# Performance work log

Hardware: AMD Instinct MI355X
Metric: run time of the kernel (lower is better)

## Reference

```python
import jax, jax.numpy as jnp
import numpy as np
import math

B, S, D, H = 4, 2048, 1024, 16
HD = D // H  # 64
SCALE = math.sqrt(HD)  # scale=True -> sqrt(d_model // n_head)

def setup_inputs() -> dict:
    key = jax.random.key(0)
    k1, k2, k3, k4, k5 = jax.random.split(key, 5)
    x = jax.random.normal(k1, (B, S, D), dtype=jnp.float32)
    char_ids = jax.random.randint(k2, (B, S), 0, 21128)
    seq_len = jax.random.randint(k3, (B,), 1, S)
    mask = jnp.ones((B, S), dtype=jnp.int64)
    W_qkv = jax.random.normal(k4, (D, 3 * D), dtype=jnp.float32) * (1.0 / math.sqrt(D))
    W_fc = jax.random.normal(k5, (D, D), dtype=jnp.float32) * (1.0 / math.sqrt(D))
    b_fc = jnp.zeros((D,), dtype=jnp.float32)
    return {"x": x, "char_ids": char_ids, "seq_len": seq_len, "mask": mask,
            "W_qkv": W_qkv, "W_fc": W_fc, "b_fc": b_fc}

def reference(x, char_ids, seq_len, mask, W_qkv, W_fc, b_fc):
    b, s, d = x.shape
    qkv = x @ W_qkv                      # [b, s, 3d]
    q, k, v = jnp.split(qkv, 3, axis=-1)
    # [b, h, s, hd]
    q = q.reshape(b, s, H, HD).transpose(0, 2, 1, 3)
    k = k.reshape(b, s, H, HD).transpose(0, 2, 1, 3)
    v = v.reshape(b, s, H, HD).transpose(0, 2, 1, 3)
    attn = jnp.einsum('bhqd,bhkd->bhqk', q, k) / SCALE
    attn = jnp.where(mask[:, None, None, :] == 0, -jnp.inf, attn)
    attn = jax.nn.softmax(attn, axis=-1)
    # dropout is identity in eval mode
    out = jnp.einsum('bhqk,bhkd->bhqd', attn, v)
    out = out.transpose(0, 2, 1, 3).reshape(b, s, d)
    return out @ W_fc + b_fc
```

## Files before the change

### kernel.cpp

```cpp
#include <hip/hip_runtime.h>
#include <hip/hip_bf16.h>


#define S_ 2048
#define D_ 1024

typedef __attribute__((ext_vector_type(4))) float f32x4;
typedef __attribute__((ext_vector_type(16))) float f32x16;
typedef __attribute__((ext_vector_type(8))) short bf16x8;

__device__ __forceinline__ unsigned short f2b(float f) {
  union { float f; unsigned u; } x; x.f = f;
  unsigned r = x.u + 0x7fffu + ((x.u >> 16) & 1u);
  return (unsigned short)(r >> 16);
}
__device__ __forceinline__ float b2f(unsigned short u) {
  union { unsigned u; float f; } x; x.u = ((unsigned)u) << 16; return x.f;
}

__device__ __forceinline__ void gload_lds16(const void* g, void* l) {
  __builtin_amdgcn_global_load_lds(
      (const __attribute__((address_space(1))) unsigned int*)g,
      (__attribute__((address_space(3))) unsigned int*)l, 16, 0, 0);
}

__global__ void cvt_f32_bf16(const float* __restrict__ in, unsigned short* __restrict__ out, int n) {
  int i = (blockIdx.x * blockDim.x + threadIdx.x) * 8;
  if (i >= n) return;
  float4 a = *(const float4*)&in[i];
  float4 b = *(const float4*)&in[i + 4];
  unsigned short r[8];
  r[0] = f2b(a.x); r[1] = f2b(a.y); r[2] = f2b(a.z); r[3] = f2b(a.w);
  r[4] = f2b(b.x); r[5] = f2b(b.y); r[6] = f2b(b.z); r[7] = f2b(b.w);
  *(uint4*)&out[i] = *(uint4*)r;
}

__global__ void transpose_cvt(const float* __restrict__ W, unsigned short* __restrict__ Wt,
                              int K, int N) {
  __shared__ unsigned short tile[32][33];
  int n0 = blockIdx.x * 32, k0 = blockIdx.y * 32;
  int tx = threadIdx.x & 31, ty = threadIdx.x >> 5;
  #pragma unroll
  for (int i = 0; i < 32; i += 8)
    tile[ty + i][tx] = f2b(W[(size_t)(k0 + ty + i) * N + n0 + tx]);
  __syncthreads();
  #pragma unroll
  for (int i = 0; i < 32; i += 8)
    Wt[(size_t)(n0 + ty + i) * K + k0 + tx] = tile[tx][ty + i];
}

template <int GY>
__global__ __launch_bounds__(256) void gemm_bt(const unsigned short* __restrict__ A,
                                               const unsigned short* __restrict__ Bt,
                                               const float* __restrict__ bias,
                                               float* __restrict__ Cf,
                                               unsigned short* __restrict__ Cb,
                                               int M, int N, int K) {
  __shared__ unsigned short As[128 * 32];
  __shared__ unsigned short Bs[128 * 32];
  int tid = threadIdx.x, wave = tid >> 6, lane = tid & 63;

  int lin = blockIdx.y * 64 + blockIdx.x;
  const int q = (GY * 64) >> 3;
  int swz = (lin & 7) * q + (lin >> 3);
  int bm = swz / GY, bn = swz % GY;

  int wr = (wave >> 1) * 64, wc = (wave & 1) * 64;
  f32x4 acc[4][4] = {};

  const unsigned short* aG0 = A + (size_t)(bm * 128 + wave * 32 + (lane >> 2)) * K + (lane & 3) * 8;
  const unsigned short* aG1 = aG0 + (size_t)16 * K;
  const unsigned short* bG0 = Bt + (size_t)(bn * 128 + wave * 32 + (lane >> 2)) * K + (lane & 3) * 8;
  const unsigned short* bG1 = bG0 + (size_t)16 * K;
  unsigned short* aL0 = As + wave * 32 * 32;
  unsigned short* aL1 = aL0 + 16 * 32;
  unsigned short* bL0 = Bs + wave * 32 * 32;
  unsigned short* bL1 = bL0 + 16 * 32;

  for (int k0 = 0; k0 < K; k0 += 32) {
    gload_lds16(aG0, aL0); gload_lds16(aG1, aL1);
    gload_lds16(bG0, bL0); gload_lds16(bG1, bL1);
    aG0 += 32; aG1 += 32; bG0 += 32; bG1 += 32;
    __syncthreads();
    bf16x8 af[4], bf[4];
    #pragma unroll
    for (int i = 0; i < 4; i++)
      af[i] = *(const bf16x8*)&As[(wr + i * 16 + (lane & 15)) * 32 + (lane >> 4) * 8];
    #pragma unroll
    for (int i = 0; i < 4; i++)
      bf[i] = *(const bf16x8*)&Bs[(wc + i * 16 + (lane & 15)) * 32 + (lane >> 4) * 8];
    #pragma unroll
    for (int i = 0; i < 4; i++)
      #pragma unroll
      for (int j = 0; j < 4; j++)
        acc[i][j] = __builtin_amdgcn_mfma_f32_16x16x32_bf16(af[i], bf[j], acc[i][j], 0, 0, 0);
    __syncthreads();
  }

  int row0 = bm * 128 + wr + (lane >> 4) * 4;
  int col0 = bn * 128 + wc + (lane & 15);
  if (Cb) {
    #pragma unroll
    for (int i = 0; i < 4; i++)
      #pragma unroll
      for (int j = 0; j < 4; j++)
        #pragma unroll
        for (int q2 = 0; q2 < 4; q2++)
          Cb[(size_t)(row0 + i * 16 + q2) * N + col0 + j * 16] = f2b(acc[i][j][q2]);
  } else {
    #pragma unroll
    for (int i = 0; i < 4; i++)
      #pragma unroll
      for (int j = 0; j < 4; j++) {
        float bv = bias[col0 + j * 16];
        #pragma unroll
        for (int q2 = 0; q2 < 4; q2++)
          Cf[(size_t)(row0 + i * 16 + q2) * N + col0 + j * 16] = acc[i][j][q2] + bv;
      }
  }
}

__global__ __launch_bounds__(256) void flash_attn(const unsigned short* __restrict__ qkv,
                                                  unsigned short* __restrict__ ao) {
  __shared__ unsigned short Ks[2][4096];
  __shared__ unsigned short Vs[2][4096];
  int tid = threadIdx.x, wave = tid >> 6, lane = tid & 63;
  int l31 = lane & 31, hi = lane >> 5;
  int bh = blockIdx.x, b = bh >> 4, h = bh & 15;
  const unsigned short* base = qkv + (size_t)b * S_ * 3072 + h * 64;
  const unsigned short* kb = base + 1024;
  const unsigned short* vb = base + 2048;
  int q0 = blockIdx.y * 256 + wave * 32;

  bf16x8 qfA[4], qfB[4];
  {
    const unsigned short* qpA = base + (size_t)(q0 + l31) * 3072 + hi * 8;
    const unsigned short* qpB = qpA + (size_t)128 * 3072;
    #pragma unroll
    for (int ks = 0; ks < 4; ks++) {
      bf16x8 va = *(const bf16x8*)(qpA + ks * 16);
      bf16x8 vc = *(const bf16x8*)(qpB + ks * 16);
      #pragma unroll
      for (int e = 0; e < 8; e++) {
        va[e] = (short)f2b(0.125f * b2f((unsigned short)va[e]));
        vc[e] = (short)f2b(0.125f * b2f((unsigned short)vc[e]));
      }
      qfA[ks] = va; qfB[ks] = vc;
    }
  }

  f32x16 oA0 = {}, oA1 = {}, oB0 = {}, oB1 = {};
  float miA = -1e30f, liA = 0.f, miB = -1e30f, liB = 0.f;

  int r_l = lane >> 3;
  int gsrc = (lane & 7) ^ r_l;
  size_t koffA = (size_t)((wave * 2 + 0) * 8 + r_l) * 3072 + gsrc * 8;
  size_t koffB = (size_t)((wave * 2 + 1) * 8 + r_l) * 3072 + gsrc * 8;
  int kvp = (tid & 31) * 2, dgr = (tid >> 5) * 8;
  int vslot = kvp >> 3;
  int vlo = kvp & 7;
  bf16x8 vr0, vr1;


  {
    gload_lds16(kb + koffA, &Ks[0][(wave * 2 + 0) * 512]);
    gload_lds16(kb + koffB, &Ks[0][(wave * 2 + 1) * 512]);
    const unsigned short* vsrc = vb + (size_t)kvp * 3072 + dgr;
    vr0 = *(const bf16x8*)vsrc;
    vr1 = *(const bf16x8*)(vsrc + 3072);
    union { bf16x8 v; unsigned u[4]; } a0, a1;
    a0.v = vr0; a1.v = vr1;
    #pragma unroll
    for (int i = 0; i < 4; i++) {
      int d0 = dgr + 2 * i, d1 = d0 + 1;
      unsigned we = (a0.u[i] & 0xffffu) | (a1.u[i] << 16);
      unsigned wo = (a0.u[i] >> 16) | (a1.u[i] & 0xffff0000u);
      *(unsigned*)&Vs[0][d0 * 64 + ((vslot ^ (d0 & 7)) << 3) + vlo] = we;
      *(unsigned*)&Vs[0][d1 * 64 + ((vslot ^ (d1 & 7)) << 3) + vlo] = wo;
    }
    __syncthreads();
  }

  for (int t = 0; t < 32; ++t) {
    int cur = t & 1;
    int tn = (t + 1) & 31;
    {
      const unsigned short* ksrc = kb + (size_t)tn * 64 * 3072;
      gload_lds16(ksrc + koffA, &Ks[cur ^ 1][(wave * 2 + 0) * 512]);
      gload_lds16(ksrc + koffB, &Ks[cur ^ 1][(wave * 2 + 1) * 512]);
      const unsigned short* vsrc = vb + (size_t)(tn * 64 + kvp) * 3072 + dgr;
      vr0 = *(const bf16x8*)vsrc;
      vr1 = *(const bf16x8*)(vsrc + 3072);
    }

    const unsigned short* Kc = Ks[cur];
    const unsigned short* Vc = Vs[cur];

    #pragma unroll
    for (int sub = 0; sub < 2; ++sub) {
      f32x16 sA = {}, sB = {};
      __builtin_amdgcn_s_setprio(1);
      #pragma unroll
      for (int ks = 0; ks < 4; ks++) {
        int row = sub * 32 + l31;
        bf16x8 kf = *(const bf16x8*)&Kc[row * 64 + ((((ks << 1) + hi) ^ (row & 7)) << 3)];
        sA = __builtin_amdgcn_mfma_f32_32x32x16_bf16(kf, qfA[ks], sA, 0, 0, 0);
        sB = __builtin_amdgcn_mfma_f32_32x32x16_bf16(kf, qfB[ks], sB, 0, 0, 0);
      }
      __builtin_amdgcn_s_setprio(0);

      union { unsigned u[4]; bf16x8 v; } PA0, PA1;
      {
        float t0 = fmaxf(fmaxf(sA[0], sA[1]), sA[2]);
        float t1 = fmaxf(fmaxf(sA[3], sA[4]), sA[5]);
        float t2 = fmaxf(fmaxf(sA[6], sA[7]), sA[8]);
        float t3 = fmaxf(fmaxf(sA[9], sA[10]), sA[11]);
        float t4 = fmaxf(fmaxf(sA[12], sA[13]), sA[14]);
        float tm = fmaxf(fmaxf(fmaxf(t0, t1), t2), fmaxf(fmaxf(t3, t4), sA[15]));
        tm = fmaxf(tm, __shfl_xor(tm, 32, 64));
        if (__any(tm > miA + 8.f)) {
          float tnew = fmaxf(miA, tm);
          float fac = __expf(miA - tnew);
          liA *= fac; miA = tnew;
          #pragma unroll
          for (int r = 0; r < 16; r++) { oA0[r] *= fac; oA1[r] *= fac; }
        }
        float p[16];
        float rs = 0.f;
        #pragma unroll
        for (int r = 0; r < 16; r++) { p[r] = __expf(sA[r] - miA); rs += p[r]; }
        liA += rs;
        unsigned c0, c1, c2, c3, c4, c5, c6, c7;
        asm("v_cvt_pk_bf16_f32 %0, %1, %2" : "=v"(c0) : "v"(p[0]),  "v"(p[1]));
        asm("v_cvt_pk_bf16_f32 %0, %1, %2" : "=v"(c1) : "v"(p[2]),  "v"(p[3]));
        asm("v_cvt_pk_bf16_f32 %0, %1, %2" : "=v"(c2) : "v"(p[4]),  "v"(p[5]));
        asm("v_cvt_pk_bf16_f32 %0, %1, %2" : "=v"(c3) : "v"(p[6]),  "v"(p[7]));
        asm("v_cvt_pk_bf16_f32 %0, %1, %2" : "=v"(c4) : "v"(p[8]),  "v"(p[9]));
        asm("v_cvt_pk_bf16_f32 %0, %1, %2" : "=v"(c5) : "v"(p[10]), "v"(p[11]));
        asm("v_cvt_pk_bf16_f32 %0, %1, %2" : "=v"(c6) : "v"(p[12]), "v"(p[13]));
        asm("v_cvt_pk_bf16_f32 %0, %1, %2" : "=v"(c7) : "v"(p[14]), "v"(p[15]));
        asm volatile("v_permlane32_swap_b32 %0, %1" : "+v"(c0), "+v"(c2));
        asm volatile("v_permlane32_swap_b32 %0, %1" : "+v"(c1), "+v"(c3));
        asm volatile("v_permlane32_swap_b32 %0, %1" : "+v"(c4), "+v"(c6));
        asm volatile("v_permlane32_swap_b32 %0, %1" : "+v"(c5), "+v"(c7));
        PA0.u[0] = c0; PA0.u[1] = c1; PA0.u[2] = c2; PA0.u[3] = c3;
        PA1.u[0] = c4; PA1.u[1] = c5; PA1.u[2] = c6; PA1.u[3] = c7;
      }
      union { unsigned u[4]; bf16x8 v; } PB0, PB1;
      {
        float t0 = fmaxf(fmaxf(sB[0], sB[1]), sB[2]);
        float t1 = fmaxf(fmaxf(sB[3], sB[4]), sB[5]);
        float t2 = fmaxf(fmaxf(sB[6], sB[7]), sB[8]);
        float t3 = fmaxf(fmaxf(sB[9], sB[10]), sB[11]);
        float t4 = fmaxf(fmaxf(sB[12], sB[13]), sB[14]);
        float tm = fmaxf(fmaxf(fmaxf(t0, t1), t2), fmaxf(fmaxf(t3, t4), sB[15]));
        tm = fmaxf(tm, __shfl_xor(tm, 32, 64));
        if (__any(tm > miB + 8.f)) {
          float tnew = fmaxf(miB, tm);
          float fac = __expf(miB - tnew);
          liB *= fac; miB = tnew;
          #pragma unroll
          for (int r = 0; r < 16; r++) { oB0[r] *= fac; oB1[r] *= fac; }
        }
        float p[16];
        float rs = 0.f;
        #pragma unroll
        for (int r = 0; r < 16; r++) { p[r] = __expf(sB[r] - miB); rs += p[r]; }
        liB += rs;
        unsigned c0, c1, c2, c3, c4, c5, c6, c7;
        asm("v_cvt_pk_bf16_f32 %0, %1, %2" : "=v"(c0) : "v"(p[0]),  "v"(p[1]));
        asm("v_cvt_pk_bf16_f32 %0, %1, %2" : "=v"(c1) : "v"(p[2]),  "v"(p[3]));
        asm("v_cvt_pk_bf16_f32 %0, %1, %2" : "=v"(c2) : "v"(p[4]),  "v"(p[5]));
        asm("v_cvt_pk_bf16_f32 %0, %1, %2" : "=v"(c3) : "v"(p[6]),  "v"(p[7]));
        asm("v_cvt_pk_bf16_f32 %0, %1, %2" : "=v"(c4) : "v"(p[8]),  "v"(p[9]));
        asm("v_cvt_pk_bf16_f32 %0, %1, %2" : "=v"(c5) : "v"(p[10]), "v"(p[11]));
        asm("v_cvt_pk_bf16_f32 %0, %1, %2" : "=v"(c6) : "v"(p[12]), "v"(p[13]));
        asm("v_cvt_pk_bf16_f32 %0, %1, %2" : "=v"(c7) : "v"(p[14]), "v"(p[15]));
        asm volatile("v_permlane32_swap_b32 %0, %1" : "+v"(c0), "+v"(c2));
        asm volatile("v_permlane32_swap_b32 %0, %1" : "+v"(c1), "+v"(c3));
        asm volatile("v_permlane32_swap_b32 %0, %1" : "+v"(c4), "+v"(c6));
        asm volatile("v_permlane32_swap_b32 %0, %1" : "+v"(c5), "+v"(c7));
        PB0.u[0] = c0; PB0.u[1] = c1; PB0.u[2] = c2; PB0.u[3] = c3;
        PB1.u[0] = c4; PB1.u[1] = c5; PB1.u[2] = c6; PB1.u[3] = c7;
      }

      int slot0 = (sub << 2) + hi;
      int slot1 = (sub << 2) + 2 + hi;
      bf16x8 v00 = *(const bf16x8*)&Vc[l31 * 64 + ((slot0 ^ (l31 & 7)) << 3)];
      bf16x8 v01 = *(const bf16x8*)&Vc[(32 + l31) * 64 + ((slot0 ^ (l31 & 7)) << 3)];
      bf16x8 v10 = *(const bf16x8*)&Vc[l31 * 64 + ((slot1 ^ (l31 & 7)) << 3)];
      bf16x8 v11 = *(const bf16x8*)&Vc[(32 + l31) * 64 + ((slot1 ^ (l31 & 7)) << 3)];
      __builtin_amdgcn_s_setprio(1);
      oA0 = __builtin_amdgcn_mfma_f32_32x32x16_bf16(v00, PA0.v, oA0, 0, 0, 0);
      oB0 = __builtin_amdgcn_mfma_f32_32x32x16_bf16(v00, PB0.v, oB0, 0, 0, 0);
      oA1 = __builtin_amdgcn_mfma_f32_32x32x16_bf16(v01, PA0.v, oA1, 0, 0, 0);
      oB1 = __builtin_amdgcn_mfma_f32_32x32x16_bf16(v01, PB0.v, oB1, 0, 0, 0);
      oA0 = __builtin_amdgcn_mfma_f32_32x32x16_bf16(v10, PA1.v, oA0, 0, 0, 0);
      oB0 = __builtin_amdgcn_mfma_f32_32x32x16_bf16(v10, PB1.v, oB0, 0, 0, 0);
      oA1 = __builtin_amdgcn_mfma_f32_32x32x16_bf16(v11, PA1.v, oA1, 0, 0, 0);
      oB1 = __builtin_amdgcn_mfma_f32_32x32x16_bf16(v11, PB1.v, oB1, 0, 0, 0);
      __builtin_amdgcn_s_setprio(0);
    }

    {
      unsigned short* Vd = Vs[cur ^ 1];
      union { bf16x8 v; unsigned u[4]; } a0, a1;
      a0.v = vr0; a1.v = vr1;
      #pragma unroll
      for (int i = 0; i < 4; i++) {
        int d0 = dgr + 2 * i, d1 = d0 + 1;
        unsigned we = (a0.u[i] & 0xffffu) | (a1.u[i] << 16);
        unsigned wo = (a0.u[i] >> 16) | (a1.u[i] & 0xffff0000u);
        *(unsigned*)&Vd[d0 * 64 + ((vslot ^ (d0 & 7)) << 3) + vlo] = we;
        *(unsigned*)&Vd[d1 * 64 + ((vslot ^ (d1 & 7)) << 3) + vlo] = wo;
      }
    }
    __syncthreads();
  }

  liA += __shfl_xor(liA, 32, 64);
  liB += __shfl_xor(liB, 32, 64);
  float invA = 1.f / liA, invB = 1.f / liB;
  unsigned short* aopA = ao + (size_t)(b * S_ + q0 + l31) * D_ + h * 64;
  unsigned short* aopB = aopA + (size_t)128 * D_;
  #pragma unroll
  for (int g = 0; g < 4; g++) {
    union { unsigned short s[4]; uint2 u; } wa0, wa1, wb0, wb1;
    #pragma unroll
    for (int e = 0; e < 4; e++) {
      wa0.s[e] = f2b(oA0[g * 4 + e] * invA);
      wa1.s[e] = f2b(oA1[g * 4 + e] * invA);
      wb0.s[e] = f2b(oB0[g * 4 + e] * invB);
      wb1.s[e] = f2b(oB1[g * 4 + e] * invB);
    }
    int d = g * 8 + hi * 4;
    *(uint2*)&aopA[d] = wa0.u;
    *(uint2*)&aopA[32 + d] = wa1.u;
    *(uint2*)&aopB[d] = wb0.u;
    *(uint2*)&aopB[32 + d] = wb1.u;
  }
}

extern "C" void kernel_launch(void* const* d_in, const int* in_sizes, int n_in,
                              void* d_out, int out_size, void* d_ws, size_t ws_size,
                              hipStream_t stream) {
  const float* x    = (const float*)d_in[0];
  const float* Wqkv = (const float*)d_in[4];
  const float* Wfc  = (const float*)d_in[5];
  const float* bfc  = (const float*)d_in[6];
  float* out = (float*)d_out;

  char* ws = (char*)d_ws;
  unsigned short* xb    = (unsigned short*)(ws);
  unsigned short* qkv   = (unsigned short*)(ws + 16777216);
  unsigned short* ao    = (unsigned short*)(ws + 67108864);
  unsigned short* wqkvT = (unsigned short*)(ws + 83886080);
  unsigned short* wfcT  = (unsigned short*)(ws + 90177536);

  cvt_f32_bf16<<<dim3(4096), dim3(256), 0, stream>>>(x, xb, 8388608);
  transpose_cvt<<<dim3(96, 32), dim3(256), 0, stream>>>(Wqkv, wqkvT, 1024, 3072);
  transpose_cvt<<<dim3(32, 32), dim3(256), 0, stream>>>(Wfc, wfcT, 1024, 1024);
  gemm_bt<24><<<dim3(64, 24), dim3(256), 0, stream>>>(xb, wqkvT, nullptr, nullptr, qkv, 8192, 3072, 1024);
  flash_attn<<<dim3(64, 8), dim3(256), 0, stream>>>(qkv, ao);
  gemm_bt<8><<<dim3(64, 8), dim3(256), 0, stream>>>(ao, wfcT, bfc, out, nullptr, 8192, 1024, 1024);
}
```

Measured before the change: 223.8 us.

## Split attention KV range across two wave groups and merge partial softmax states

The flash attention block grows to 512 threads. Two groups of four waves each process half of the key/value sequence for the same query rows, and their partial outputs and max/sum statistics are combined through shared memory at the end. Softmax exponentials now use exp2 with a prescaled max. The GEMM drops its tile-order swizzle in favour of plain blockIdx mapping, which may hurt L2 locality. The aim is more waves in flight per query tile and a shorter serial KV loop, at the cost of twice the LDS per block and an extra merge step.

After: 410.9 us. +83.6%, slower.

```diff
diff --git a/kernel.cpp b/kernel.cpp
--- a/kernel.cpp
+++ b/kernel.cpp
@@ -49,7 +49,6 @@
     Wt[(size_t)(n0 + ty + i) * K + k0 + tx] = tile[tx][ty + i];
 }
 
-template <int GY>
 __global__ __launch_bounds__(256) void gemm_bt(const unsigned short* __restrict__ A,
                                                const unsigned short* __restrict__ Bt,
                                                const float* __restrict__ bias,
@@ -59,12 +58,7 @@
   __shared__ unsigned short As[128 * 32];
   __shared__ unsigned short Bs[128 * 32];
   int tid = threadIdx.x, wave = tid >> 6, lane = tid & 63;
-
-  int lin = blockIdx.y * 64 + blockIdx.x;
-  const int q = (GY * 64) >> 3;
-  int swz = (lin & 7) * q + (lin >> 3);
-  int bm = swz / GY, bn = swz % GY;
-
+  int bm = blockIdx.x, bn = blockIdx.y;
   int wr = (wave >> 1) * 64, wc = (wave & 1) * 64;
   f32x4 acc[4][4] = {};
 
@@ -105,8 +99,8 @@
       #pragma unroll
       for (int j = 0; j < 4; j++)
         #pragma unroll
-        for (int q2 = 0; q2 < 4; q2++)
-          Cb[(size_t)(row0 + i * 16 + q2) * N + col0 + j * 16] = f2b(acc[i][j][q2]);
+        for (int q = 0; q < 4; q++)
+          Cb[(size_t)(row0 + i * 16 + q) * N + col0 + j * 16] = f2b(acc[i][j][q]);
   } else {
     #pragma unroll
     for (int i = 0; i < 4; i++)
@@ -114,23 +108,27 @@
       for (int j = 0; j < 4; j++) {
         float bv = bias[col0 + j * 16];
         #pragma unroll
-        for (int q2 = 0; q2 < 4; q2++)
-          Cf[(size_t)(row0 + i * 16 + q2) * N + col0 + j * 16] = acc[i][j][q2] + bv;
-      }
-  }
-}
-
-__global__ __launch_bounds__(256) void flash_attn(const unsigned short* __restrict__ qkv,
-                                                  unsigned short* __restrict__ ao) {
-  __shared__ unsigned short Ks[2][4096];
-  __shared__ unsigned short Vs[2][4096];
+        for (int q = 0; q < 4; q++)
+          Cf[(size_t)(row0 + i * 16 + q) * N + col0 + j * 16] = acc[i][j][q] + bv;
+      }
+  }
+}
+
+__global__ __launch_bounds__(512, 4) void flash_attn(const unsigned short* __restrict__ qkv,
+                                                     unsigned short* __restrict__ ao) {
+  __shared__ unsigned short Ks[2][2][4096];
+  __shared__ unsigned short Vs[2][2][4096];
+  __shared__ float mstat[4][32][4];
+  const float L2E = 1.4426950408889634f;
   int tid = threadIdx.x, wave = tid >> 6, lane = tid & 63;
+  int half = wave >> 2, w4 = wave & 3;
+  int tid256 = tid & 255;
   int l31 = lane & 31, hi = lane >> 5;
   int bh = blockIdx.x, b = bh >> 4, h = bh & 15;
   const unsigned short* base = qkv + (size_t)b * S_ * 3072 + h * 64;
-  const unsigned short* kb = base + 1024;
-  const unsigned short* vb = base + 2048;
-  int q0 = blockIdx.y * 256 + wave * 32;
+  const unsigned short* kb = base + 1024 + (size_t)(half * 16) * 64 * 3072;
+  const unsigned short* vb = base + 2048 + (size_t)(half * 16) * 64 * 3072;
+  int q0 = blockIdx.y * 256 + w4 * 32;
 
   bf16x8 qfA[4], qfB[4];
   {
@@ -150,21 +148,21 @@
   }
 
   f32x16 oA0 = {}, oA1 = {}, oB0 = {}, oB1 = {};
-  float miA = -1e30f, liA = 0.f, miB = -1e30f, liB = 0.f;
+  float miA = -1e30f, miAL = -1.442695e30f, liA = 0.f;
+  float miB = -1e30f, miBL = -1.442695e30f, liB = 0.f;
 
   int r_l = lane >> 3;
   int gsrc = (lane & 7) ^ r_l;
-  size_t koffA = (size_t)((wave * 2 + 0) * 8 + r_l) * 3072 + gsrc * 8;
-  size_t koffB = (size_t)((wave * 2 + 1) * 8 + r_l) * 3072 + gsrc * 8;
-  int kvp = (tid & 31) * 2, dgr = (tid >> 5) * 8;
+  size_t koffA = (size_t)((w4 * 2 + 0) * 8 + r_l) * 3072 + gsrc * 8;
+  size_t koffB = (size_t)((w4 * 2 + 1) * 8 + r_l) * 3072 + gsrc * 8;
+  int kvp = (tid256 & 31) * 2, dgr = (tid256 >> 5) * 8;
   int vslot = kvp >> 3;
   int vlo = kvp & 7;
   bf16x8 vr0, vr1;
 
-
   {
-    gload_lds16(kb + koffA, &Ks[0][(wave * 2 + 0) * 512]);
-    gload_lds16(kb + koffB, &Ks[0][(wave * 2 + 1) * 512]);
+    gload_lds16(kb + koffA, &Ks[half][0][(w4 * 2 + 0) * 512]);
+    gload_lds16(kb + koffB, &Ks[half][0][(w4 * 2 + 1) * 512]);
     const unsigned short* vsrc = vb + (size_t)kvp * 3072 + dgr;
     vr0 = *(const bf16x8*)vsrc;
     vr1 = *(const bf16x8*)(vsrc + 3072);
@@ -175,26 +173,26 @@
       int d0 = dgr + 2 * i, d1 = d0 + 1;
       unsigned we = (a0.u[i] & 0xffffu) | (a1.u[i] << 16);
       unsigned wo = (a0.u[i] >> 16) | (a1.u[i] & 0xffff0000u);
-      *(unsigned*)&Vs[0][d0 * 64 + ((vslot ^ (d0 & 7)) << 3) + vlo] = we;
-      *(unsigned*)&Vs[0][d1 * 64 + ((vslot ^ (d1 & 7)) << 3) + vlo] = wo;
+      *(unsigned*)&Vs[half][0][d0 * 64 + ((vslot ^ (d0 & 7)) << 3) + vlo] = we;
+      *(unsigned*)&Vs[half][0][d1 * 64 + ((vslot ^ (d1 & 7)) << 3) + vlo] = wo;
     }
     __syncthreads();
   }
 
-  for (int t = 0; t < 32; ++t) {
-    int cur = t & 1;
-    int tn = (t + 1) & 31;
-    {
+  for (int tt = 0; tt < 16; ++tt) {
+    int cur = tt & 1;
+    if (tt < 15) {
+      int tn = tt + 1;
       const unsigned short* ksrc = kb + (size_t)tn * 64 * 3072;
-      gload_lds16(ksrc + koffA, &Ks[cur ^ 1][(wave * 2 + 0) * 512]);
-      gload_lds16(ksrc + koffB, &Ks[cur ^ 1][(wave * 2 + 1) * 512]);
+      gload_lds16(ksrc + koffA, &Ks[half][cur ^ 1][(w4 * 2 + 0) * 512]);
+      gload_lds16(ksrc + koffB, &Ks[half][cur ^ 1][(w4 * 2 + 1) * 512]);
       const unsigned short* vsrc = vb + (size_t)(tn * 64 + kvp) * 3072 + dgr;
       vr0 = *(const bf16x8*)vsrc;
       vr1 = *(const bf16x8*)(vsrc + 3072);
     }
 
-    const unsigned short* Kc = Ks[cur];
-    const unsigned short* Vc = Vs[cur];
+    const unsigned short* Kc = Ks[half][cur];
+    const unsigned short* Vc = Vs[half][cur];
 
     #pragma unroll
     for (int sub = 0; sub < 2; ++sub) {
@@ -220,15 +218,16 @@
         tm = fmaxf(tm, __shfl_xor(tm, 32, 64));
         if (__any(tm > miA + 8.f)) {
           float tnew = fmaxf(miA, tm);
-          float fac = __expf(miA - tnew);
-          liA *= fac; miA = tnew;
+          float tL = tnew * L2E;
+          float fac = exp2f(miAL - tL);
+          liA *= fac; miA = tnew; miAL = tL;
           #pragma unroll
           for (int r = 0; r < 16; r++) { oA0[r] *= fac; oA1[r] *= fac; }
         }
         float p[16];
         float rs = 0.f;
         #pragma unroll
-        for (int r = 0; r < 16; r++) { p[r] = __expf(sA[r] - miA); rs += p[r]; }
+        for (int r = 0; r < 16; r++) { p[r] = exp2f(fmaf(sA[r], L2E, -miAL)); rs += p[r]; }
         liA += rs;
         unsigned c0, c1, c2, c3, c4, c5, c6, c7;
         asm("v_cvt_pk_bf16_f32 %0, %1, %2" : "=v"(c0) : "v"(p[0]),  "v"(p[1]));
@@ -257,15 +256,16 @@
         tm = fmaxf(tm, __shfl_xor(tm, 32, 64));
         if (__any(tm > miB + 8.f)) {
           float tnew = fmaxf(miB, tm);
-          float fac = __expf(miB - tnew);
-          liB *= fac; miB = tnew;
+          float tL = tnew * L2E;
+          float fac = exp2f(miBL - tL);
+          liB *= fac; miB = tnew; miBL = tL;
           #pragma unroll
           for (int r = 0; r < 16; r++) { oB0[r] *= fac; oB1[r] *= fac; }
         }
         float p[16];
         float rs = 0.f;
         #pragma unroll
-        for (int r = 0; r < 16; r++) { p[r] = __expf(sB[r] - miB); rs += p[r]; }
+        for (int r = 0; r < 16; r++) { p[r] = exp2f(fmaf(sB[r], L2E, -miBL)); rs += p[r]; }
         liB += rs;
         unsigned c0, c1, c2, c3, c4, c5, c6, c7;
         asm("v_cvt_pk_bf16_f32 %0, %1, %2" : "=v"(c0) : "v"(p[0]),  "v"(p[1]));
@@ -302,8 +302,8 @@
       __builtin_amdgcn_s_setprio(0);
     }
 
-    {
-      unsigned short* Vd = Vs[cur ^ 1];
+    if (tt < 15) {
+      unsigned short* Vd = Vs[half][cur ^ 1];
       union { bf16x8 v; unsigned u[4]; } a0, a1;
       a0.v = vr0; a1.v = vr1;
       #pragma unroll
@@ -320,24 +320,52 @@
 
   liA += __shfl_xor(liA, 32, 64);
   liB += __shfl_xor(liB, 32, 64);
-  float invA = 1.f / liA, invB = 1.f / liB;
-  unsigned short* aopA = ao + (size_t)(b * S_ + q0 + l31) * D_ + h * 64;
-  unsigned short* aopB = aopA + (size_t)128 * D_;
-  #pragma unroll
-  for (int g = 0; g < 4; g++) {
-    union { unsigned short s[4]; uint2 u; } wa0, wa1, wb0, wb1;
-    #pragma unroll
-    for (int e = 0; e < 4; e++) {
-      wa0.s[e] = f2b(oA0[g * 4 + e] * invA);
-      wa1.s[e] = f2b(oA1[g * 4 + e] * invA);
-      wb0.s[e] = f2b(oB0[g * 4 + e] * invB);
-      wb1.s[e] = f2b(oB1[g * 4 + e] * invB);
-    }
-    int d = g * 8 + hi * 4;
-    *(uint2*)&aopA[d] = wa0.u;
-    *(uint2*)&aopA[32 + d] = wa1.u;
-    *(uint2*)&aopB[d] = wb0.u;
-    *(uint2*)&aopB[32 + d] = wb1.u;
+
+  float* obufA = (float*)&Ks[0][0][0];
+  float* obufB = (float*)&Vs[0][0][0];
+  if (half == 1) {
+    if (lane < 32) {
+      mstat[w4][l31][0] = miA; mstat[w4][l31][1] = liA;
+      mstat[w4][l31][2] = miB; mstat[w4][l31][3] = liB;
+    }
+    int idx = (w4 * 64 + lane) * 32;
+    #pragma unroll
+    for (int j = 0; j < 16; j++) { obufA[idx + j] = oA0[j]; obufA[idx + 16 + j] = oA1[j]; }
+    #pragma unroll
+    for (int j = 0; j < 16; j++) { obufB[idx + j] = oB0[j]; obufB[idx + 16 + j] = oB1[j]; }
+  }
+  __syncthreads();
+
+  if (half == 0) {
+    float mA1 = mstat[w4][l31][0], lA1 = mstat[w4][l31][1];
+    float mB1 = mstat[w4][l31][2], lB1 = mstat[w4][l31][3];
+    float mA = fmaxf(miA, mA1), mB = fmaxf(miB, mB1);
+    float fA0 = __expf(miA - mA), fA1 = __expf(mA1 - mA);
+    float fB0 = __expf(miB - mB), fB1 = __expf(mB1 - mB);
+    float invA = 1.f / (liA * fA0 + lA1 * fA1);
+    float invB = 1.f / (liB * fB0 + lB1 * fB1);
+    float gA0 = fA0 * invA, gA1 = fA1 * invA;
+    float gB0 = fB0 * invB, gB1 = fB1 * invB;
+    int idx = (w4 * 64 + lane) * 32;
+    unsigned short* aopA = ao + (size_t)(b * S_ + q0 + l31) * D_ + h * 64;
+    unsigned short* aopB = aopA + (size_t)128 * D_;
+    #pragma unroll
+    for (int g = 0; g < 4; g++) {
+      union { unsigned short s[4]; uint2 u; } wa0, wa1, wb0, wb1;
+      #pragma unroll
+      for (int e = 0; e < 4; e++) {
+        int j = g * 4 + e;
+        wa0.s[e] = f2b(oA0[j] * gA0 + obufA[idx + j] * gA1);
+        wa1.s[e] = f2b(oA1[j] * gA0 + obufA[idx + 16 + j] * gA1);
+        wb0.s[e] = f2b(oB0[j] * gB0 + obufB[idx + j] * gB1);
+        wb1.s[e] = f2b(oB1[j] * gB0 + obufB[idx + 16 + j] * gB1);
+      }
+      int d = g * 8 + hi * 4;
+      *(uint2*)&aopA[d] = wa0.u;
+      *(uint2*)&aopA[32 + d] = wa1.u;
+      *(uint2*)&aopB[d] = wb0.u;
+      *(uint2*)&aopB[32 + d] = wb1.u;
+    }
   }
 }
 
@@ -360,7 +388,7 @@
   cvt_f32_bf16<<<dim3(4096), dim3(256), 0, stream>>>(x, xb, 8388608);
   transpose_cvt<<<dim3(96, 32), dim3(256), 0, stream>>>(Wqkv, wqkvT, 1024, 3072);
   transpose_cvt<<<dim3(32, 32), dim3(256), 0, stream>>>(Wfc, wfcT, 1024, 1024);
-  gemm_bt<24><<<dim3(64, 24), dim3(256), 0, stream>>>(xb, wqkvT, nullptr, nullptr, qkv, 8192, 3072, 1024);
-  flash_attn<<<dim3(64, 8), dim3(256), 0, stream>>>(qkv, ao);
-  gemm_bt<8><<<dim3(64, 8), dim3(256), 0, stream>>>(ao, wfcT, bfc, out, nullptr, 8192, 1024, 1024);
-}
+  gemm_bt<<<dim3(64, 24), dim3(256), 0, stream>>>(xb, wqkvT, nullptr, nullptr, qkv, 8192, 3072, 1024);
+  flash_attn<<<dim3(64, 8), dim3(512), 0, stream>>>(qkv, ao);
+  gemm_bt<<<dim3(64, 8), dim3(256), 0, stream>>>(ao, wfcT, bfc, out, nullptr, 8192, 1024, 1024);
+}
```

## Triple-buffer GEMM LDS tiles with explicit waitcnt pipelining and drop block swizzle

Applied to the files above, without the earlier changes.

The bf16 GEMM moves from a single LDS buffer with load-then-sync per K step to a three-stage ring. Global-to-LDS loads for tile k+2 are issued while MFMAs run on tile k, and hand-written s_waitcnt vmcnt/s_barrier sequences replace __syncthreads. This aims to hide global load latency behind matrix math. The K loop is now hard-coded for K=1024 (32 tiles). The grouped block-index swizzle is removed in favour of a direct blockIdx mapping, which may reduce L2 reuse between neighbouring workgroups.

After: 219.9 us (median of 2 runs). Within noise of the previous version (-1.7%).

```diff
diff --git a/kernel.cpp b/kernel.cpp
--- a/kernel.cpp
+++ b/kernel.cpp
@@ -49,53 +49,90 @@
     Wt[(size_t)(n0 + ty + i) * K + k0 + tx] = tile[tx][ty + i];
 }
 
-template <int GY>
 __global__ __launch_bounds__(256) void gemm_bt(const unsigned short* __restrict__ A,
                                                const unsigned short* __restrict__ Bt,
                                                const float* __restrict__ bias,
                                                float* __restrict__ Cf,
                                                unsigned short* __restrict__ Cb,
                                                int M, int N, int K) {
-  __shared__ unsigned short As[128 * 32];
-  __shared__ unsigned short Bs[128 * 32];
+  __shared__ unsigned short As[3][128 * 32];
+  __shared__ unsigned short Bs[3][128 * 32];
   int tid = threadIdx.x, wave = tid >> 6, lane = tid & 63;
-
-  int lin = blockIdx.y * 64 + blockIdx.x;
-  const int q = (GY * 64) >> 3;
-  int swz = (lin & 7) * q + (lin >> 3);
-  int bm = swz / GY, bn = swz % GY;
-
+  int bm = blockIdx.x, bn = blockIdx.y;
   int wr = (wave >> 1) * 64, wc = (wave & 1) * 64;
   f32x4 acc[4][4] = {};
 
-  const unsigned short* aG0 = A + (size_t)(bm * 128 + wave * 32 + (lane >> 2)) * K + (lane & 3) * 8;
-  const unsigned short* aG1 = aG0 + (size_t)16 * K;
-  const unsigned short* bG0 = Bt + (size_t)(bn * 128 + wave * 32 + (lane >> 2)) * K + (lane & 3) * 8;
-  const unsigned short* bG1 = bG0 + (size_t)16 * K;
-  unsigned short* aL0 = As + wave * 32 * 32;
-  unsigned short* aL1 = aL0 + 16 * 32;
-  unsigned short* bL0 = Bs + wave * 32 * 32;
-  unsigned short* bL1 = bL0 + 16 * 32;
-
-  for (int k0 = 0; k0 < K; k0 += 32) {
-    gload_lds16(aG0, aL0); gload_lds16(aG1, aL1);
-    gload_lds16(bG0, bL0); gload_lds16(bG1, bL1);
-    aG0 += 32; aG1 += 32; bG0 += 32; bG1 += 32;
-    __syncthreads();
-    bf16x8 af[4], bf[4];
-    #pragma unroll
-    for (int i = 0; i < 4; i++)
-      af[i] = *(const bf16x8*)&As[(wr + i * 16 + (lane & 15)) * 32 + (lane >> 4) * 8];
-    #pragma unroll
-    for (int i = 0; i < 4; i++)
-      bf[i] = *(const bf16x8*)&Bs[(wc + i * 16 + (lane & 15)) * 32 + (lane >> 4) * 8];
-    #pragma unroll
-    for (int i = 0; i < 4; i++)
-      #pragma unroll
-      for (int j = 0; j < 4; j++)
-        acc[i][j] = __builtin_amdgcn_mfma_f32_16x16x32_bf16(af[i], bf[j], acc[i][j], 0, 0, 0);
-    __syncthreads();
-  }
+  const unsigned short* aBase = A + (size_t)(bm * 128 + wave * 32 + (lane >> 2)) * K + (lane & 3) * 8;
+  const unsigned short* bBase = Bt + (size_t)(bn * 128 + wave * 32 + (lane >> 2)) * K + (lane & 3) * 8;
+  const size_t row16 = (size_t)16 * K;
+  int ldst0 = wave * 1024 + lane * 8;
+  int ldst1 = ldst0 + 512;
+
+  #define STAGE_G(kt, sb)                                                      \
+    do {                                                                       \
+      const unsigned short* ap = aBase + (kt) * 32;                            \
+      const unsigned short* bp = bBase + (kt) * 32;                            \
+      gload_lds16(ap, &As[sb][ldst0]);                                         \
+      gload_lds16(ap + row16, &As[sb][ldst1]);                                 \
+      gload_lds16(bp, &Bs[sb][ldst0]);                                         \
+      gload_lds16(bp + row16, &Bs[sb][ldst1]);                                 \
+    } while (0)
+
+  #define READ_MFMA_G(sb)                                                      \
+    do {                                                                       \
+      bf16x8 af[4], bf[4];                                                     \
+      _Pragma("unroll")                                                        \
+      for (int i = 0; i < 4; i++)                                              \
+        af[i] = *(const bf16x8*)&As[sb][(wr + i * 16 + (lane & 15)) * 32 + (lane >> 4) * 8]; \
+      _Pragma("unroll")                                                        \
+      for (int i = 0; i < 4; i++)                                              \
+        bf[i] = *(const bf16x8*)&Bs[sb][(wc + i * 16 + (lane & 15)) * 32 + (lane >> 4) * 8]; \
+      _Pragma("unroll")                                                        \
+      for (int i = 0; i < 4; i++)                                              \
+        _Pragma("unroll")                                                      \
+        for (int j = 0; j < 4; j++)                                            \
+          acc[i][j] = __builtin_amdgcn_mfma_f32_16x16x32_bf16(af[i], bf[j], acc[i][j], 0, 0, 0); \
+    } while (0)
+
+  #define TRAIL_SYNC()                                                         \
+    do {                                                                       \
+      asm volatile("s_waitcnt lgkmcnt(0)" ::: "memory");                       \
+      asm volatile("s_barrier" ::: "memory");                                  \
+    } while (0)
+
+  STAGE_G(0, 0);
+  STAGE_G(1, 1);
+  asm volatile("s_waitcnt vmcnt(4)" ::: "memory");
+  asm volatile("s_barrier" ::: "memory");
+
+  for (int t3 = 0; t3 < 10; ++t3) {
+    int kt = t3 * 3;
+    STAGE_G(kt + 2, 2);
+    asm volatile("s_waitcnt vmcnt(8)" ::: "memory");
+    asm volatile("s_barrier" ::: "memory");
+    READ_MFMA_G(0);
+    TRAIL_SYNC();
+    STAGE_G(kt + 3, 0);
+    asm volatile("s_waitcnt vmcnt(8)" ::: "memory");
+    asm volatile("s_barrier" ::: "memory");
+    READ_MFMA_G(1);
+    TRAIL_SYNC();
+    STAGE_G(kt + 4, 1);
+    asm volatile("s_waitcnt vmcnt(8)" ::: "memory");
+    asm volatile("s_barrier" ::: "memory");
+    READ_MFMA_G(2);
+    TRAIL_SYNC();
+  }
+  asm volatile("s_waitcnt vmcnt(4)" ::: "memory");
+  asm volatile("s_barrier" ::: "memory");
+  READ_MFMA_G(0);
+  TRAIL_SYNC();
+  asm volatile("s_waitcnt vmcnt(0)" ::: "memory");
+  asm volatile("s_barrier" ::: "memory");
+  READ_MFMA_G(1);
+  #undef STAGE_G
+  #undef READ_MFMA_G
+  #undef TRAIL_SYNC
 
   int row0 = bm * 128 + wr + (lane >> 4) * 4;
   int col0 = bn * 128 + wc + (lane & 15);
@@ -105,8 +142,8 @@
       #pragma unroll
       for (int j = 0; j < 4; j++)
         #pragma unroll
-        for (int q2 = 0; q2 < 4; q2++)
-          Cb[(size_t)(row0 + i * 16 + q2) * N + col0 + j * 16] = f2b(acc[i][j][q2]);
+        for (int q = 0; q < 4; q++)
+          Cb[(size_t)(row0 + i * 16 + q) * N + col0 + j * 16] = f2b(acc[i][j][q]);
   } else {
     #pragma unroll
     for (int i = 0; i < 4; i++)
@@ -114,8 +151,8 @@
       for (int j = 0; j < 4; j++) {
         float bv = bias[col0 + j * 16];
         #pragma unroll
-        for (int q2 = 0; q2 < 4; q2++)
-          Cf[(size_t)(row0 + i * 16 + q2) * N + col0 + j * 16] = acc[i][j][q2] + bv;
+        for (int q = 0; q < 4; q++)
+          Cf[(size_t)(row0 + i * 16 + q) * N + col0 + j * 16] = acc[i][j][q] + bv;
       }
   }
 }
@@ -160,7 +197,6 @@
   int vslot = kvp >> 3;
   int vlo = kvp & 7;
   bf16x8 vr0, vr1;
-
 
   {
     gload_lds16(kb + koffA, &Ks[0][(wave * 2 + 0) * 512]);
@@ -360,7 +396,7 @@
   cvt_f32_bf16<<<dim3(4096), dim3(256), 0, stream>>>(x, xb, 8388608);
   transpose_cvt<<<dim3(96, 32), dim3(256), 0, stream>>>(Wqkv, wqkvT, 1024, 3072);
   transpose_cvt<<<dim3(32, 32), dim3(256), 0, stream>>>(Wfc, wfcT, 1024, 1024);
-  gemm_bt<24><<<dim3(64, 24), dim3(256), 0, stream>>>(xb, wqkvT, nullptr, nullptr, qkv, 8192, 3072, 1024);
+  gemm_bt<<<dim3(64, 24), dim3(256), 0, stream>>>(xb, wqkvT, nullptr, nullptr, qkv, 8192, 3072, 1024);
   flash_attn<<<dim3(64, 8), dim3(256), 0, stream>>>(qkv, ao);
-  gemm_bt<8><<<dim3(64, 8), dim3(256), 0, stream>>>(ao, wfcT, bfc, out, nullptr, 8192, 1024, 1024);
-}
+  gemm_bt<<<dim3(64, 8), dim3(256), 0, stream>>>(ao, wfcT, bfc, out, nullptr, 8192, 1024, 1024);
+}
```
